# Kernel optimization log

Measured on AMD Instinct MI355X. Metric: run time of the kernel, lower is better.

## Reference

```python
import jax, jax.numpy as jnp
import numpy as np

B, T, C = 4, 2048, 1024
N_HEAD = 16
HEAD = C // N_HEAD  # 64


def _rope_tables(T, dim, base=10000.0):
    inv_freq = 1.0 / (base ** (jnp.arange(0, dim, 2, dtype=jnp.float32) / dim))
    t = jnp.arange(T, dtype=jnp.float32)
    freqs = jnp.einsum('i,j->ij', t, inv_freq)           # [T, dim/2]
    emb = jnp.concatenate([freqs, freqs], axis=-1)        # [T, dim]
    return jnp.cos(emb), jnp.sin(emb)                     # each [T, dim]


def _rotate_half(x):
    x1, x2 = x[..., : x.shape[-1] // 2], x[..., x.shape[-1] // 2:]
    return jnp.concatenate([-x2, x1], axis=-1)


def setup_inputs() -> dict:
    key = jax.random.key(0)
    ks = jax.random.split(key, 4)
    x = jax.random.normal(ks[0], (B, T, C), dtype=jnp.float32)
    w_attn = jax.random.normal(ks[1], (C, 3 * C), dtype=jnp.float32) * (1.0 / np.sqrt(C))
    b_attn = jnp.zeros((3 * C,), dtype=jnp.float32)
    w_proj = jax.random.normal(ks[2], (C, C), dtype=jnp.float32) * (1.0 / np.sqrt(C))
    b_proj = jnp.zeros((C,), dtype=jnp.float32)
    return {"x": x, "w_attn": w_attn, "b_attn": b_attn, "w_proj": w_proj, "b_proj": b_proj}


def reference(x, w_attn, b_attn, w_proj, b_proj):
    Bx, Tx, Cx = x.shape
    qkv = x @ w_attn + b_attn                             # [B,T,3C]
    q, k, v = jnp.split(qkv, 3, axis=-1)
    # [B,T,C] -> [B,H,T,hd]
    def to_heads(t):
        return t.reshape(Bx, Tx, N_HEAD, HEAD).transpose(0, 2, 1, 3)
    q, k, v = to_heads(q), to_heads(k), to_heads(v)
    cos, sin = _rope_tables(Tx, HEAD)                     # [T,hd]
    cos = cos[None, None, :, :]
    sin = sin[None, None, :, :]
    q = q * cos + _rotate_half(q) * sin
    k = k * cos + _rotate_half(k) * sin
    scale = 1.0 / np.sqrt(HEAD)
    att = jnp.einsum('bhqd,bhkd->bhqk', q, k) * scale     # [B,H,T,T]
    causal = jnp.tril(jnp.ones((Tx, Tx), dtype=bool))
    att = jnp.where(causal[None, None], att, -jnp.inf)
    att = jax.nn.softmax(att, axis=-1)
    y = jnp.einsum('bhqk,bhkd->bhqd', att, v)             # [B,H,T,hd]
    y = y.transpose(0, 2, 1, 3).reshape(Bx, Tx, Cx)
    return y @ w_proj + b_proj
```

## Files before the change

kernel.cpp:

```cpp
#include <hip/hip_runtime.h>

#define B_  4
#define T_  2048
#define C_  1024
#define NH_ 16
#define HD_ 64
#define BT_ (B_*T_)
#define N3C (3*C_)

typedef _Float16 f16;
typedef _Float16 half8 __attribute__((ext_vector_type(8)));
typedef _Float16 half4 __attribute__((ext_vector_type(4)));
typedef float f32x4 __attribute__((ext_vector_type(4)));

__device__ __forceinline__ void gld16(const f16* g, f16* l) {
  __builtin_amdgcn_global_load_lds(
      (const __attribute__((address_space(1))) unsigned int*)g,
      (__attribute__((address_space(3))) unsigned int*)l, 16, 0, 0);
}

__global__ __launch_bounds__(256) void cvt_x(const float* __restrict__ X,
                                             f16* __restrict__ X16)
{
  const int i = blockIdx.x * 256 + threadIdx.x;
  const float4 a = ((const float4*)X)[i * 2];
  const float4 b = ((const float4*)X)[i * 2 + 1];
  half8 h;
  h[0] = (f16)a.x; h[1] = (f16)a.y; h[2] = (f16)a.z; h[3] = (f16)a.w;
  h[4] = (f16)b.x; h[5] = (f16)b.y; h[6] = (f16)b.z; h[7] = (f16)b.w;
  ((half8*)X16)[i] = h;
}

__global__ __launch_bounds__(256) void cvt_transpose(
    const float* __restrict__ W, f16* __restrict__ Wt, int K, int N)
{
  __shared__ float Ls[64][65];
  const int tid = threadIdx.x;
  const int n0 = blockIdx.x * 64, k0 = blockIdx.y * 64;
#pragma unroll
  for (int j = 0; j < 4; ++j) {
    const int idx = j * 256 + tid;
    const int r = idx >> 4, c = (idx & 15) * 4;
    const float4 w = *(const float4*)(W + (size_t)(k0 + r) * N + n0 + c);
    Ls[r][c + 0] = w.x; Ls[r][c + 1] = w.y; Ls[r][c + 2] = w.z; Ls[r][c + 3] = w.w;
  }
  __syncthreads();
#pragma unroll
  for (int j = 0; j < 2; ++j) {
    const int idx = j * 256 + tid;
    const int r = idx >> 3, c = (idx & 7) * 8;
    half8 h;
#pragma unroll
    for (int u = 0; u < 8; ++u) h[u] = (f16)Ls[c + u][r];
    *(half8*)(Wt + (size_t)(n0 + r) * K + k0 + c) = h;
  }
}

__global__ __launch_bounds__(256) void gemm_qkv(
    const f16* __restrict__ A, const f16* __restrict__ Bt,
    const float* __restrict__ bias,
    f16* __restrict__ Qo, f16* __restrict__ Ko, f16* __restrict__ Vt_g)
{
  __shared__ f16 As[128 * 32];
  __shared__ f16 Bs[128 * 32];
  const int tid  = threadIdx.x;
  const int row0 = blockIdx.y * 128;
  const int col0 = blockIdx.x * 128;
  const int wave = tid >> 6, lane = tid & 63;
  const int l = lane & 15, quad = lane >> 4;
  const int wm = wave >> 1, wn = wave & 1;
  const int sr = tid >> 2, sc = (tid & 3) * 8;

  f32x4 acc[4][4];
#pragma unroll
  for (int mi = 0; mi < 4; ++mi)
#pragma unroll
    for (int ni = 0; ni < 4; ++ni) acc[mi][ni] = (f32x4)0.0f;

  for (int k0 = 0; k0 < C_; k0 += 32) {
    __syncthreads();
#pragma unroll
    for (int p = 0; p < 2; ++p) {
      gld16(A  + (size_t)(row0 + p * 64 + sr) * C_ + k0 + sc, &As[p * 2048 + tid * 8]);
      gld16(Bt + (size_t)(col0 + p * 64 + sr) * C_ + k0 + sc, &Bs[p * 2048 + tid * 8]);
    }
    __syncthreads();

    half8 af[4], bf[4];
#pragma unroll
    for (int mi = 0; mi < 4; ++mi)
      af[mi] = *(const half8*)&As[(wm * 64 + mi * 16 + l) * 32 + quad * 8];
#pragma unroll
    for (int ni = 0; ni < 4; ++ni)
      bf[ni] = *(const half8*)&Bs[(wn * 64 + ni * 16 + l) * 32 + quad * 8];
#pragma unroll
    for (int mi = 0; mi < 4; ++mi)
#pragma unroll
      for (int ni = 0; ni < 4; ++ni)
        acc[mi][ni] = __builtin_amdgcn_mfma_f32_16x16x32_f16(af[mi], bf[ni], acc[mi][ni], 0, 0, 0);
  }

  const int region = col0 >> 10;
  const int colw = col0 + wn * 64;
  const int h = (colw & 1023) >> 6;
  if (region < 2) {
    f16* dst = (region == 0) ? Qo : Ko;
#pragma unroll
    for (int mi = 0; mi < 4; ++mi) {
#pragma unroll
      for (int ni = 0; ni < 4; ++ni) {
#pragma unroll
        for (int r = 0; r < 4; ++r) {
          const int gm = row0 + wm * 64 + mi * 16 + quad * 4 + r;
          const int b = gm >> 11, t = gm & (T_ - 1);
          const int d = ni * 16 + l;
          const float val = acc[mi][ni][r] + bias[colw + d];
          dst[((size_t)(b * NH_ + h) * T_ + t) * HD_ + d] = (f16)val;
        }
      }
    }
  } else {
#pragma unroll
    for (int mi = 0; mi < 4; ++mi) {
      const int t0 = row0 + wm * 64 + mi * 16 + quad * 4;
      const int b = t0 >> 11, t = t0 & (T_ - 1);
#pragma unroll
      for (int ni = 0; ni < 4; ++ni) {
        const int d = ni * 16 + l;
        const float bs = bias[colw + d];
        half4 o;
#pragma unroll
        for (int r = 0; r < 4; ++r) o[r] = (f16)(acc[mi][ni][r] + bs);
        *(half4*)(Vt_g + ((size_t)((b * NH_ + h) * HD_ + d)) * T_ + t) = o;
      }
    }
  }
}

__global__ __launch_bounds__(256) void rope_qk(f16* __restrict__ Q,
                                               f16* __restrict__ Ko)
{
  const int idx = blockIdx.x * 256 + threadIdx.x;
  const int f   = idx & 31;
  const int row = idx >> 5;
  const int t   = row & (T_ - 1);
  const float e   = (float)(2 * f) * (1.0f / 64.0f);
  const float inv = expf(-e * 9.210340371976184f);
  const float ang = (float)t * inv;
  float sn, cn;
  sincosf(ang, &sn, &cn);

  const size_t p = (size_t)row * HD_ + f;
  {
    float x1 = (float)Q[p], x2 = (float)Q[p + 32];
    Q[p]      = (f16)(x1 * cn - x2 * sn);
    Q[p + 32] = (f16)(x2 * cn + x1 * sn);
  }
  {
    float x1 = (float)Ko[p], x2 = (float)Ko[p + 32];
    Ko[p]      = (f16)(x1 * cn - x2 * sn);
    Ko[p + 32] = (f16)(x2 * cn + x1 * sn);
  }
}

__global__ __launch_bounds__(256) void attn_mfma(
    const f16* __restrict__ Qg, const f16* __restrict__ Kg,
    const f16* __restrict__ Vt_g, f16* __restrict__ Y)
{
  __shared__ f16 Ks[64 * 64];
  __shared__ f16 Vt[64 * 64];
  const int tid  = threadIdx.x;
  const int qt   = 31 - (blockIdx.x >> 6);
  const int bh   = blockIdx.x & 63;
  const int b    = bh >> 4, h = bh & 15;
  const int wave = tid >> 6, lane = tid & 63;
  const int l    = lane & 15, quad = lane >> 4;
  const int qrow = qt * 64 + wave * 16 + l;

  const f16* qp = Qg + ((size_t)bh * T_ + qrow) * HD_;
  half8 qf[2];
#pragma unroll
  for (int s = 0; s < 2; ++s)
    qf[s] = *(const half8*)(qp + s * 32 + quad * 8);

  f32x4 O[4];
#pragma unroll
  for (int mi = 0; mi < 4; ++mi) O[mi] = (f32x4)0.0f;
  float m_run = -1e30f, l_run = 0.f;

  const f16* kbase  = Kg   + (size_t)bh * T_ * HD_;
  const f16* vtbase = Vt_g + (size_t)bh * HD_ * T_;
  const int lq7 = l & 7;

  for (int kt = 0; kt <= qt; ++kt) {
    __syncthreads();
#pragma unroll
    for (int i = 0; i < 2; ++i) {
      const int r = i * 32 + (tid >> 3);
      const int c = tid & 7;
      const int cs = ((c ^ (r & 7)) << 3);
      const half8 hk = *(const half8*)(kbase + (size_t)(kt * 64 + r) * HD_ + c * 8);
      *(half8*)&Ks[r * 64 + cs] = hk;
      const half8 hv = *(const half8*)(vtbase + (size_t)r * T_ + kt * 64 + c * 8);
      *(half8*)&Vt[r * 64 + cs] = hv;
    }
    __syncthreads();

    f32x4 St[4];
#pragma unroll
    for (int st = 0; st < 4; ++st) {
      f32x4 s_acc = (f32x4)0.0f;
#pragma unroll
      for (int s = 0; s < 2; ++s) {
        const int row = st * 16 + l;
        const half8 af = *(const half8*)&Ks[row * 64 + ((((s << 2) | quad) ^ lq7) << 3)];
        s_acc = __builtin_amdgcn_mfma_f32_16x16x32_f16(af, qf[s], s_acc, 0, 0, 0);
      }
      St[st] = s_acc;
    }

    float p[4][4];
    float cmax = -1e30f;
    const bool diag = (kt == qt);
#pragma unroll
    for (int st = 0; st < 4; ++st)
#pragma unroll
      for (int r = 0; r < 4; ++r) {
        float x = St[st][r] * 0.125f;
        if (diag) {
          const int key = kt * 64 + st * 16 + quad * 4 + r;
          if (key > qrow) x = -1e9f;
        }
        p[st][r] = x;
        cmax = fmaxf(cmax, x);
      }
    cmax = fmaxf(cmax, __shfl_xor(cmax, 16));
    cmax = fmaxf(cmax, __shfl_xor(cmax, 32));
    const float mnew  = fmaxf(m_run, cmax);
    const float alpha = __expf(m_run - mnew);
    float psum = 0.f;
#pragma unroll
    for (int st = 0; st < 4; ++st)
#pragma unroll
      for (int r = 0; r < 4; ++r) {
        const float ev = __expf(p[st][r] - mnew);
        p[st][r] = ev;
        psum += ev;
      }
    psum += __shfl_xor(psum, 16);
    psum += __shfl_xor(psum, 32);
    l_run = l_run * alpha + psum;
    m_run = mnew;

    half4 pf[4];
#pragma unroll
    for (int st = 0; st < 4; ++st) {
      pf[st][0] = (f16)p[st][0]; pf[st][1] = (f16)p[st][1];
      pf[st][2] = (f16)p[st][2]; pf[st][3] = (f16)p[st][3];
      O[st] *= alpha;
    }

#pragma unroll
    for (int mi = 0; mi < 4; ++mi) {
      const int row = mi * 16 + l;
#pragma unroll
      for (int ki = 0; ki < 4; ++ki) {
        const int kch = (ki << 1) | (quad >> 1);
        const half4 vf = *(const half4*)&Vt[row * 64 + ((kch ^ lq7) << 3) + ((quad & 1) << 2)];
        O[mi] = __builtin_amdgcn_mfma_f32_16x16x16f16(vf, pf[ki], O[mi], 0, 0, 0);
      }
    }
  }

  const float inv = 1.0f / l_run;
  f16* yp = Y + ((size_t)(b * T_) + qrow) * C_ + h * 64;
#pragma unroll
  for (int mi = 0; mi < 4; ++mi) {
    half4 o;
    o[0] = (f16)(O[mi][0] * inv); o[1] = (f16)(O[mi][1] * inv);
    o[2] = (f16)(O[mi][2] * inv); o[3] = (f16)(O[mi][3] * inv);
    *(half4*)(yp + mi * 16 + quad * 4) = o;
  }
}

__global__ __launch_bounds__(256) void gemm_proj(
    const f16* __restrict__ A, const f16* __restrict__ Bt,
    const float* __restrict__ bias, float* __restrict__ Out)
{
  __shared__ f16 As[128 * 32];
  __shared__ f16 Bs[128 * 32];
  const int tid  = threadIdx.x;
  const int row0 = blockIdx.y * 128;
  const int col0 = blockIdx.x * 128;
  const int wave = tid >> 6, lane = tid & 63;
  const int l = lane & 15, quad = lane >> 4;
  const int wm = wave >> 1, wn = wave & 1;
  const int sr = tid >> 2, sc = (tid & 3) * 8;

  f32x4 acc[4][4];
#pragma unroll
  for (int mi = 0; mi < 4; ++mi)
#pragma unroll
    for (int ni = 0; ni < 4; ++ni) acc[mi][ni] = (f32x4)0.0f;

  for (int k0 = 0; k0 < C_; k0 += 32) {
    __syncthreads();
#pragma unroll
    for (int p = 0; p < 2; ++p) {
      gld16(A  + (size_t)(row0 + p * 64 + sr) * C_ + k0 + sc, &As[p * 2048 + tid * 8]);
      gld16(Bt + (size_t)(col0 + p * 64 + sr) * C_ + k0 + sc, &Bs[p * 2048 + tid * 8]);
    }
    __syncthreads();

    half8 af[4], bf[4];
#pragma unroll
    for (int mi = 0; mi < 4; ++mi)
      af[mi] = *(const half8*)&As[(wm * 64 + mi * 16 + l) * 32 + quad * 8];
#pragma unroll
    for (int ni = 0; ni < 4; ++ni)
      bf[ni] = *(const half8*)&Bs[(wn * 64 + ni * 16 + l) * 32 + quad * 8];
#pragma unroll
    for (int mi = 0; mi < 4; ++mi)
#pragma unroll
      for (int ni = 0; ni < 4; ++ni)
        acc[mi][ni] = __builtin_amdgcn_mfma_f32_16x16x32_f16(af[mi], bf[ni], acc[mi][ni], 0, 0, 0);
  }

#pragma unroll
  for (int mi = 0; mi < 4; ++mi) {
#pragma unroll
    for (int ni = 0; ni < 4; ++ni) {
#pragma unroll
      for (int r = 0; r < 4; ++r) {
        const int gm = row0 + wm * 64 + mi * 16 + quad * 4 + r;
        const int n  = col0 + wn * 64 + ni * 16 + l;
        Out[(size_t)gm * C_ + n] = acc[mi][ni][r] + bias[n];
      }
    }
  }
}

extern "C" void kernel_launch(void* const* d_in, const int* in_sizes, int n_in,
                              void* d_out, int out_size, void* d_ws, size_t ws_size,
                              hipStream_t stream) {
  const float* x      = (const float*)d_in[0];
  const float* w_attn = (const float*)d_in[1];
  const float* b_attn = (const float*)d_in[2];
  const float* w_proj = (const float*)d_in[3];
  const float* b_proj = (const float*)d_in[4];
  float* out = (float*)d_out;

  const size_t elems = (size_t)BT_ * C_;
  f16* x16 = (f16*)d_ws;
  f16* wta = x16 + elems;
  f16* wtp = wta + (size_t)N3C * C_;
  f16* q   = wtp + (size_t)C_ * C_;
  f16* k   = q + elems;
  f16* vt  = k + elems;
  f16* y   = vt + elems;

  cvt_x<<<dim3(elems / 8 / 256), 256, 0, stream>>>(x, x16);
  cvt_transpose<<<dim3(N3C / 64, C_ / 64), 256, 0, stream>>>(w_attn, wta, C_, N3C);
  cvt_transpose<<<dim3(C_ / 64, C_ / 64), 256, 0, stream>>>(w_proj, wtp, C_, C_);
  gemm_qkv<<<dim3(N3C / 128, BT_ / 128), 256, 0, stream>>>(x16, wta, b_attn, q, k, vt);
  rope_qk<<<dim3((B_ * NH_ * T_ * 32) / 256), 256, 0, stream>>>(q, k);
  attn_mfma<<<dim3(32 * 64), 256, 0, stream>>>(q, k, vt, y);
  gemm_proj<<<dim3(C_ / 128, BT_ / 128), 256, 0, stream>>>(y, wtp, b_proj, out);
}
```

Before: 290.0 us.

## Fuse RoPE into QKV GEMM epilogue and widen K-tile with XOR-swizzled LDS

Result: faster. 277.5 us (-4.3%).

```diff
diff --git a/kernel.cpp b/kernel.cpp
--- a/kernel.cpp
+++ b/kernel.cpp
@@ -61,15 +61,17 @@
     const float* __restrict__ bias,
     f16* __restrict__ Qo, f16* __restrict__ Ko, f16* __restrict__ Vt_g)
 {
-  __shared__ f16 As[128 * 32];
-  __shared__ f16 Bs[128 * 32];
+  __shared__ f16 As[128 * 64];
+  __shared__ f16 Bs[128 * 64];
   const int tid  = threadIdx.x;
   const int row0 = blockIdx.y * 128;
   const int col0 = blockIdx.x * 128;
   const int wave = tid >> 6, lane = tid & 63;
   const int l = lane & 15, quad = lane >> 4;
   const int wm = wave >> 1, wn = wave & 1;
-  const int sr = tid >> 2, sc = (tid & 3) * 8;
+  const int sr = tid >> 3;
+  const int scs = ((tid & 7) ^ (sr & 7)) * 8;
+  const int lq7 = l & 7;
 
   f32x4 acc[4][4];
 #pragma unroll
@@ -77,27 +79,31 @@
 #pragma unroll
     for (int ni = 0; ni < 4; ++ni) acc[mi][ni] = (f32x4)0.0f;
 
-  for (int k0 = 0; k0 < C_; k0 += 32) {
-    __syncthreads();
-#pragma unroll
-    for (int p = 0; p < 2; ++p) {
-      gld16(A  + (size_t)(row0 + p * 64 + sr) * C_ + k0 + sc, &As[p * 2048 + tid * 8]);
-      gld16(Bt + (size_t)(col0 + p * 64 + sr) * C_ + k0 + sc, &Bs[p * 2048 + tid * 8]);
-    }
-    __syncthreads();
-
-    half8 af[4], bf[4];
-#pragma unroll
-    for (int mi = 0; mi < 4; ++mi)
-      af[mi] = *(const half8*)&As[(wm * 64 + mi * 16 + l) * 32 + quad * 8];
-#pragma unroll
-    for (int ni = 0; ni < 4; ++ni)
-      bf[ni] = *(const half8*)&Bs[(wn * 64 + ni * 16 + l) * 32 + quad * 8];
-#pragma unroll
-    for (int mi = 0; mi < 4; ++mi)
+  for (int k0 = 0; k0 < C_; k0 += 64) {
+    __syncthreads();
+#pragma unroll
+    for (int p = 0; p < 4; ++p) {
+      const int r = p * 32 + sr;
+      gld16(A  + (size_t)(row0 + r) * C_ + k0 + scs, &As[p * 2048 + tid * 8]);
+      gld16(Bt + (size_t)(col0 + r) * C_ + k0 + scs, &Bs[p * 2048 + tid * 8]);
+    }
+    __syncthreads();
+
+#pragma unroll
+    for (int s = 0; s < 2; ++s) {
+      half8 af[4], bf[4];
+#pragma unroll
+      for (int mi = 0; mi < 4; ++mi)
+        af[mi] = *(const half8*)&As[(wm * 64 + mi * 16 + l) * 64 + ((((s << 2) | quad) ^ lq7) << 3)];
 #pragma unroll
       for (int ni = 0; ni < 4; ++ni)
-        acc[mi][ni] = __builtin_amdgcn_mfma_f32_16x16x32_f16(af[mi], bf[ni], acc[mi][ni], 0, 0, 0);
+        bf[ni] = *(const half8*)&Bs[(wn * 64 + ni * 16 + l) * 64 + ((((s << 2) | quad) ^ lq7) << 3)];
+#pragma unroll
+      for (int mi = 0; mi < 4; ++mi)
+#pragma unroll
+        for (int ni = 0; ni < 4; ++ni)
+          acc[mi][ni] = __builtin_amdgcn_mfma_f32_16x16x32_f16(af[mi], bf[ni], acc[mi][ni], 0, 0, 0);
+    }
   }
 
   const int region = col0 >> 10;
@@ -105,17 +111,28 @@
   const int h = (colw & 1023) >> 6;
   if (region < 2) {
     f16* dst = (region == 0) ? Qo : Ko;
+    float invf[2];
+#pragma unroll
+    for (int ni = 0; ni < 2; ++ni) {
+      const float fr = (float)(ni * 16 + l);
+      invf[ni] = expf(-(2.0f * fr / 64.0f) * 9.210340371976184f);
+    }
 #pragma unroll
     for (int mi = 0; mi < 4; ++mi) {
 #pragma unroll
-      for (int ni = 0; ni < 4; ++ni) {
-#pragma unroll
-        for (int r = 0; r < 4; ++r) {
-          const int gm = row0 + wm * 64 + mi * 16 + quad * 4 + r;
-          const int b = gm >> 11, t = gm & (T_ - 1);
+      for (int r = 0; r < 4; ++r) {
+        const int gm = row0 + wm * 64 + mi * 16 + quad * 4 + r;
+        const int b = gm >> 11, t = gm & (T_ - 1);
+        const size_t base = ((size_t)(b * NH_ + h) * T_ + t) * HD_;
+#pragma unroll
+        for (int ni = 0; ni < 2; ++ni) {
           const int d = ni * 16 + l;
-          const float val = acc[mi][ni][r] + bias[colw + d];
-          dst[((size_t)(b * NH_ + h) * T_ + t) * HD_ + d] = (f16)val;
+          const float x1 = acc[mi][ni][r]     + bias[colw + d];
+          const float x2 = acc[mi][ni + 2][r] + bias[colw + d + 32];
+          float sn, cn;
+          sincosf((float)t * invf[ni], &sn, &cn);
+          dst[base + d]      = (f16)(x1 * cn - x2 * sn);
+          dst[base + d + 32] = (f16)(x2 * cn + x1 * sn);
         }
       }
     }
@@ -134,32 +151,6 @@
         *(half4*)(Vt_g + ((size_t)((b * NH_ + h) * HD_ + d)) * T_ + t) = o;
       }
     }
-  }
-}
-
-__global__ __launch_bounds__(256) void rope_qk(f16* __restrict__ Q,
-                                               f16* __restrict__ Ko)
-{
-  const int idx = blockIdx.x * 256 + threadIdx.x;
-  const int f   = idx & 31;
-  const int row = idx >> 5;
-  const int t   = row & (T_ - 1);
-  const float e   = (float)(2 * f) * (1.0f / 64.0f);
-  const float inv = expf(-e * 9.210340371976184f);
-  const float ang = (float)t * inv;
-  float sn, cn;
-  sincosf(ang, &sn, &cn);
-
-  const size_t p = (size_t)row * HD_ + f;
-  {
-    float x1 = (float)Q[p], x2 = (float)Q[p + 32];
-    Q[p]      = (f16)(x1 * cn - x2 * sn);
-    Q[p + 32] = (f16)(x2 * cn + x1 * sn);
-  }
-  {
-    float x1 = (float)Ko[p], x2 = (float)Ko[p + 32];
-    Ko[p]      = (f16)(x1 * cn - x2 * sn);
-    Ko[p + 32] = (f16)(x2 * cn + x1 * sn);
   }
 }
 
@@ -287,15 +278,17 @@
     const f16* __restrict__ A, const f16* __restrict__ Bt,
     const float* __restrict__ bias, float* __restrict__ Out)
 {
-  __shared__ f16 As[128 * 32];
-  __shared__ f16 Bs[128 * 32];
+  __shared__ f16 As[128 * 64];
+  __shared__ f16 Bs[128 * 64];
   const int tid  = threadIdx.x;
   const int row0 = blockIdx.y * 128;
   const int col0 = blockIdx.x * 128;
   const int wave = tid >> 6, lane = tid & 63;
   const int l = lane & 15, quad = lane >> 4;
   const int wm = wave >> 1, wn = wave & 1;
-  const int sr = tid >> 2, sc = (tid & 3) * 8;
+  const int sr = tid >> 3;
+  const int scs = ((tid & 7) ^ (sr & 7)) * 8;
+  const int lq7 = l & 7;
 
   f32x4 acc[4][4];
 #pragma unroll
@@ -303,27 +296,31 @@
 #pragma unroll
     for (int ni = 0; ni < 4; ++ni) acc[mi][ni] = (f32x4)0.0f;
 
-  for (int k0 = 0; k0 < C_; k0 += 32) {
-    __syncthreads();
-#pragma unroll
-    for (int p = 0; p < 2; ++p) {
-      gld16(A  + (size_t)(row0 + p * 64 + sr) * C_ + k0 + sc, &As[p * 2048 + tid * 8]);
-      gld16(Bt + (size_t)(col0 + p * 64 + sr) * C_ + k0 + sc, &Bs[p * 2048 + tid * 8]);
-    }
-    __syncthreads();
-
-    half8 af[4], bf[4];
-#pragma unroll
-    for (int mi = 0; mi < 4; ++mi)
-      af[mi] = *(const half8*)&As[(wm * 64 + mi * 16 + l) * 32 + quad * 8];
-#pragma unroll
-    for (int ni = 0; ni < 4; ++ni)
-      bf[ni] = *(const half8*)&Bs[(wn * 64 + ni * 16 + l) * 32 + quad * 8];
-#pragma unroll
-    for (int mi = 0; mi < 4; ++mi)
+  for (int k0 = 0; k0 < C_; k0 += 64) {
+    __syncthreads();
+#pragma unroll
+    for (int p = 0; p < 4; ++p) {
+      const int r = p * 32 + sr;
+      gld16(A  + (size_t)(row0 + r) * C_ + k0 + scs, &As[p * 2048 + tid * 8]);
+      gld16(Bt + (size_t)(col0 + r) * C_ + k0 + scs, &Bs[p * 2048 + tid * 8]);
+    }
+    __syncthreads();
+
+#pragma unroll
+    for (int s = 0; s < 2; ++s) {
+      half8 af[4], bf[4];
+#pragma unroll
+      for (int mi = 0; mi < 4; ++mi)
+        af[mi] = *(const half8*)&As[(wm * 64 + mi * 16 + l) * 64 + ((((s << 2) | quad) ^ lq7) << 3)];
 #pragma unroll
       for (int ni = 0; ni < 4; ++ni)
-        acc[mi][ni] = __builtin_amdgcn_mfma_f32_16x16x32_f16(af[mi], bf[ni], acc[mi][ni], 0, 0, 0);
+        bf[ni] = *(const half8*)&Bs[(wn * 64 + ni * 16 + l) * 64 + ((((s << 2) | quad) ^ lq7) << 3)];
+#pragma unroll
+      for (int mi = 0; mi < 4; ++mi)
+#pragma unroll
+        for (int ni = 0; ni < 4; ++ni)
+          acc[mi][ni] = __builtin_amdgcn_mfma_f32_16x16x32_f16(af[mi], bf[ni], acc[mi][ni], 0, 0, 0);
+    }
   }
 
 #pragma unroll
@@ -363,7 +360,6 @@
   cvt_transpose<<<dim3(N3C / 64, C_ / 64), 256, 0, stream>>>(w_attn, wta, C_, N3C);
   cvt_transpose<<<dim3(C_ / 64, C_ / 64), 256, 0, stream>>>(w_proj, wtp, C_, C_);
   gemm_qkv<<<dim3(N3C / 128, BT_ / 128), 256, 0, stream>>>(x16, wta, b_attn, q, k, vt);
-  rope_qk<<<dim3((B_ * NH_ * T_ * 32) / 256), 256, 0, stream>>>(q, k);
   attn_mfma<<<dim3(32 * 64), 256, 0, stream>>>(q, k, vt, y);
   gemm_proj<<<dim3(C_ / 128, BT_ / 128), 256, 0, stream>>>(y, wtp, b_proj, out);
 }
```
